# Performance work log

Measured on AMD Instinct MI355X. Metric: run time of the kernel, lower is better.

## Reference

```python
import jax, jax.numpy as jnp
from jax import lax
import numpy as np


def hac_round(X, W):
    """Avg-linkage HAC build+cut rounding of fractional SDP matrix X (D,D).
    Returns the 0/1 symmetric round_matrix with 1-diagonal."""
    D = X.shape[0]
    dt = X.dtype
    MAXD = jnp.max(jnp.abs(X)) * 1000.0  # _MAX_DIST sentinel
    max_sim = jnp.max(X)                 # max_similarity passed by forward()
    tril_mask = jnp.tril(jnp.ones((D, D), dtype=bool))
    # use_similarities=True branch: Y = MAXD*tril + (max_sim - X).triu(1)
    Y = jnp.where(tril_mask, MAXD, max_sim - X)
    values = jnp.min(Y, axis=1)
    indices = jnp.argmin(Y, axis=1)
    parents = jnp.arange(2 * D - 1)
    p2i = jnp.arange(2 * D - 1)   # parent_to_idx
    i2p = jnp.arange(D)           # idx_to_parent
    cs = jnp.ones(2 * D - 1, dtype=dt)
    energy = jnp.zeros(2 * D - 1, dtype=dt)
    clustering = jnp.zeros((2 * D - 1, D), dtype=dt)
    clustering = clustering.at[jnp.arange(D), jnp.arange(D)].set(jnp.arange(1, D + 1, dtype=dt))
    R = jnp.eye(D, dtype=dt)

    def body(i, st):
        Y, values, indices, parents, p2i, i2p, cs, energy, clustering, R = st
        max_node = D + i
        m1 = jnp.argmin(values)
        m2 = indices[m1]
        p1 = i2p[p2i[i2p[m1]]]
        p2 = i2p[p2i[i2p[m2]]]
        parents = parents.at[p1].set(max_node).at[p2].set(max_node)
        i2p = i2p.at[m1].set(max_node)
        p2i = p2i.at[max_node].set(m1)
        max_mask = Y == MAXD
        cs1, cs2 = cs[p1], cs[p2]
        ncs = cs1 + cs2
        cs = cs.at[max_node].set(ncs)
        # weighted average-linkage merged distances
        newv = (jnp.minimum(Y[m1, :], Y[:, m1]) * cs1 + jnp.minimum(Y[:, m2], Y[m2, :]) * cs2) / ncs
        Y = Y.at[:, m1].set(newv).at[m1, :].set(newv)
        Y = jnp.where(max_mask, MAXD, Y)
        Y = Y.at[:, m2].set(MAXD).at[m2, :].set(MAXD)
        values = values.at[m2].set(MAXD)
        vmask = values == MAXD
        values = jnp.where(vmask, MAXD, jnp.min(Y, axis=1))
        indices = jnp.argmin(Y, axis=1)
        # cut decision for the new internal node
        crow = clustering[p1] + clustering[p2]
        leaf = crow > 0                      # membership of new cluster
        lf = leaf.astype(dt)
        merge_e = lf @ (W @ lf)              # sum of W over leaf x leaf pairs
        e_sum = energy[p1] + energy[p2]
        take = merge_e >= e_sum
        energy = energy.at[max_node].set(jnp.where(take, merge_e, e_sum))
        crow = jnp.where(take & leaf, (max_node).astype(dt), crow)
        clustering = clustering.at[max_node].set(crow)
        R = jnp.where(take & (leaf[:, None] & leaf[None, :]), jnp.asarray(1.0, dt), R)
        return (Y, values, indices, parents, p2i, i2p, cs, energy, clustering, R)

    st = (Y, values, indices, parents, p2i, i2p, cs, energy, clustering, R)
    st = lax.fori_loop(0, D - 1, body, st)
    return st[-1]


def setup_inputs() -> dict:
    key = jax.random.key(0)
    k1, k2 = jax.random.split(key)
    D = 1024
    A = jax.random.uniform(k1, (D, D), dtype=jnp.float32)
    X = 0.5 * (A + A.T)                      # symmetric fractional decisions
    X = X.at[jnp.arange(D), jnp.arange(D)].set(1.0)  # 1-diagonal
    W = jnp.triu(jax.random.normal(k2, (D, D), dtype=jnp.float32), 1)  # triu(1) weights
    return {"X": X, "W": W}


def reference(X, W):
    # straight-through estimator: hard rounded solution, identity gradient w.r.t. X
    R = hac_round(X, W)
    return X + lax.stop_gradient(R - X)
```

## Files before the change

### kernel.cpp

```cpp
#include <hip/hip_runtime.h>
#include <stdint.h>

#define D 1024

typedef unsigned long long u64;
typedef unsigned int u32;

__device__ __forceinline__ u32 enc_f(float f) {
    u32 b = __float_as_uint(f);
    return (b & 0x80000000u) ? ~b : (b | 0x80000000u);
}
__device__ __forceinline__ float dec_f(u32 u) {
    u32 b = (u & 0x80000000u) ? (u ^ 0x80000000u) : ~u;
    return __uint_as_float(b);
}

__device__ __forceinline__ void barrier_lds_only() {
    __builtin_amdgcn_sched_barrier(0);
    asm volatile("s_waitcnt lgkmcnt(0)" ::: "memory");
    __builtin_amdgcn_s_barrier();
    asm volatile("" ::: "memory");
    __builtin_amdgcn_sched_barrier(0);
}

__global__ void k_maxred(const float* __restrict__ X, u32* scal) {
    float mx = -INFINITY, ma = 0.f;
    int stride = gridDim.x * blockDim.x;
    for (int i = blockIdx.x * blockDim.x + threadIdx.x; i < D * D; i += stride) {
        float v = X[i];
        mx = fmaxf(mx, v);
        ma = fmaxf(ma, fabsf(v));
    }
    for (int o = 32; o; o >>= 1) {
        mx = fmaxf(mx, __shfl_xor(mx, o));
        ma = fmaxf(ma, __shfl_xor(ma, o));
    }
    if ((threadIdx.x & 63) == 0) {
        atomicMax(&scal[0], enc_f(mx));
        atomicMax(&scal[1], enc_f(ma));
    }
}

__global__ void k_init(const float* __restrict__ X, const float* __restrict__ W,
                       float2* __restrict__ dc, const u32* __restrict__ scal) {
    int idx = blockIdx.x * blockDim.x + threadIdx.x;
    if (idx >= D * D) return;
    float max_sim = dec_f(scal[0]);
    float MAXD = __fmul_rn(dec_f(scal[1]), 1000.0f);
    int i = idx >> 10, j = idx & (D - 1);
    float x = X[idx];
    float di = (i == j) ? MAXD : __fsub_rn(max_sim, x);
    float cx = (i == j) ? 0.0f : (W[idx] + W[j * D + i]);
    dc[idx] = make_float2(di, cx);
}

__global__ void k_rowmin(const float2* __restrict__ dc, float* __restrict__ values_g,
                         int* __restrict__ indices_g, const u32* __restrict__ scal) {
    int r = blockIdx.x;
    int lane = threadIdx.x;
    float MAXD = __fmul_rn(dec_f(scal[1]), 1000.0f);
    u64 best = ((u64)__float_as_uint(MAXD) << 32);
    const float4* row4 = (const float4*)(dc + (size_t)r * D);
    for (int c = lane; c < D / 2; c += 64) {
        float4 q = row4[c];
        int j0 = c << 1;
        if (j0 > r) {
            u64 k = ((u64)__float_as_uint(q.x) << 32) | (u32)j0;
            if (k < best) best = k;
        }
        if (j0 + 1 > r) {
            u64 k = ((u64)__float_as_uint(q.z) << 32) | (u32)(j0 + 1);
            if (k < best) best = k;
        }
    }
    for (int o = 32; o; o >>= 1) {
        u64 k2 = __shfl_xor(best, o);
        if (k2 < best) best = k2;
    }
    if (lane == 0) {
        values_g[r] = __uint_as_float((u32)(best >> 32));
        indices_g[r] = (int)(best & 0xffffffffu);
    }
}

__global__ void __launch_bounds__(1024) k_hac(
        float2* __restrict__ dc,
        const float* __restrict__ values_g, const int* __restrict__ indices_g,
        int* __restrict__ labels_g, const u32* __restrict__ scal) {
    __shared__ __align__(16) float values_l[D];
    __shared__ float values_stage[D];
    __shared__ int indices_l[D];
    __shared__ __align__(16) float newv_l[D];
    __shared__ float cs_l[D];
    __shared__ unsigned char dead_l[D];
    __shared__ unsigned char marked_l[D];
    __shared__ int slot_l[D];
    __shared__ int label_l[D];
    __shared__ double within_l[D];
    __shared__ double energy_l[D];
    __shared__ int rlist[2][D];
    __shared__ int nrec[2];
    __shared__ u64 s_best[2];
    __shared__ float s_cross12;
    __shared__ int s_takeP, s_m1P, s_labP;

    const int t = threadIdx.x;
    const int lane = t & 63, wid = t >> 6;
    const float MAXD = __fmul_rn(dec_f(scal[1]), 1000.0f);
    const u32 MAXDb = __float_as_uint(MAXD);

    values_l[t] = values_g[t];
    indices_l[t] = indices_g[t];
    cs_l[t] = 1.0f;
    dead_l[t] = 0;
    marked_l[t] = 0;
    slot_l[t] = t;
    label_l[t] = t;
    within_l[t] = 0.0;
    energy_l[t] = 0.0;
    if (t == 0) {
        s_takeP = 0; s_m1P = -1; s_labP = 0;
        nrec[0] = 0; nrec[1] = 0;
        s_best[0] = ~0ull; s_best[1] = ~0ull;
    }
    __syncthreads();
    {
        u64 key = ((u64)__float_as_uint(values_l[t]) << 32) | ((u32)t << 10) |
                  (u32)indices_l[t];
        for (int o = 32; o; o >>= 1) {
            u64 k2 = __shfl_xor(key, o);
            if (k2 < key) key = k2;
        }
        if (lane == 0) atomicMin(&s_best[0], key);
    }
    __syncthreads();

    float pf0 = 0.f, pf1 = 0.f, pf2 = 0.f, pf3 = 0.f;

    for (int it = 0; it < D - 1; ++it) {
        const int cb = it & 1, pb = cb ^ 1;

        const u64 bk = s_best[cb];
        const int m1 = (int)((bk >> 10) & 1023);
        const int m2 = (int)(bk & 1023);

        const float2 v1 = dc[(size_t)m1 * D + t];
        const float2 v2 = dc[(size_t)m2 * D + t];

        const float cs1 = cs_l[m1], cs2 = cs_l[m2];
        const float ncs = __fadd_rn(cs1, cs2);
        const int pm1 = s_m1P;
        const int takeP = s_takeP, labP = s_labP;
        if (t == 0) s_best[pb] = ~0ull;

        if (marked_l[t]) { values_l[t] = values_stage[t]; marked_l[t] = 0; }
        if (t == m2) {
            dead_l[m2] = 1;
            values_l[m2] = MAXD;
            indices_l[m2] = 0;
        }
        const bool alive = !dead_l[t];

        const float d1 = v1.x, c1 = v1.y, d2 = v2.x, c2 = v2.y;

        {
            int sl = slot_l[t];
            if (takeP && sl == pm1) label_l[t] = labP;
            if (sl == m2) slot_l[t] = m1;
        }

        float nv = MAXD, ncx = 0.0f;
        bool do_st = false;
        if (t == m2) s_cross12 = c1;
        if (alive && t != m1) {
            nv = __fdiv_rn(__fadd_rn(__fmul_rn(d1, cs1), __fmul_rn(d2, cs2)), ncs);
            ncx = c1 + c2;
            dc[(size_t)m1 * D + t] = make_float2(nv, ncx);
            do_st = true;
        }
        newv_l[t] = nv;

        {
            float v = values_l[t];
            if (t == m1) {
                values_l[t] = MAXD;
                marked_l[t] = 1;
            } else if (alive && v < MAXD) {
                int idx = indices_l[t];
                if (idx == m2) {
                    rlist[cb][atomicAdd(&nrec[cb], 1)] = t;
                    values_l[t] = MAXD;
                    marked_l[t] = 1;
                } else if (idx == m1) {
                    if (nv <= v) values_l[t] = nv;
                    else {
                        rlist[cb][atomicAdd(&nrec[cb], 1)] = t;
                        values_l[t] = MAXD;
                        marked_l[t] = 1;
                    }
                } else if (t < m1) {
                    if (nv < v) { values_l[t] = nv; indices_l[t] = m1; }
                    else if (nv == v && m1 < idx) indices_l[t] = m1;
                }
            }
        }
        barrier_lds_only();

        if (t == m1) cs_l[m1] = ncs;
        const int n = nrec[cb];
        if (t == 0) nrec[pb] = 0;

        if (wid == 0) {
            if (do_st) dc[(size_t)t * D + m1] = make_float2(nv, ncx);
            if (lane == 0) {
                double merge_e = within_l[m1] + within_l[m2] + (double)s_cross12;
                double e_sum = energy_l[m1] + energy_l[m2];
                int take = (merge_e >= e_sum) ? 1 : 0;
                within_l[m1] = merge_e;
                energy_l[m1] = take ? merge_e : e_sum;
                s_takeP = take;
                s_m1P = m1;
                s_labP = D + it;
            }
            const float4* v4 = (const float4*)values_l;
            u64 bb = ~0ull;
#pragma unroll
            for (int c = 0; c < 4; ++c) {
                int fi = lane + 64 * c;
                float4 q = v4[fi];
                int b = fi << 2;
                u64 k;
                k = ((u64)__float_as_uint(q.x) << 32) | (u32)(b + 0); if (k < bb) bb = k;
                k = ((u64)__float_as_uint(q.y) << 32) | (u32)(b + 1); if (k < bb) bb = k;
                k = ((u64)__float_as_uint(q.z) << 32) | (u32)(b + 2); if (k < bb) bb = k;
                k = ((u64)__float_as_uint(q.w) << 32) | (u32)(b + 3); if (k < bb) bb = k;
            }
            for (int o = 32; o; o >>= 1) {
                u64 k2 = __shfl_xor(bb, o);
                if (k2 < bb) bb = k2;
            }
            if (lane == 0) {
                int r = (int)(bb & 1023);
                int idx = indices_l[r];
                atomicMin(&s_best[pb],
                          (bb & 0xffffffff00000000ull) | ((u32)r << 10) | (u32)idx);
            }
            {
                int r_pf = (int)(bb & 1023);
                int i_pf = indices_l[r_pf];
                const float* br = (const float*)(dc + (size_t)r_pf * D);
                const float* bi = (const float*)(dc + (size_t)i_pf * D);
                pf0 = br[lane * 16];
                pf1 = br[1024 + lane * 16];
                pf2 = bi[lane * 16];
                pf3 = bi[1024 + lane * 16];
            }
        } else if (wid == 1) {
            if (do_st) dc[(size_t)t * D + m1] = make_float2(nv, ncx);
            u64 bb = ((u64)MAXDb << 32);
            const float4* nv4 = (const float4*)newv_l;
            for (int c = lane; c < D / 4; c += 64) {
                float4 q = nv4[c];
                int j0 = c << 2;
#pragma unroll
                for (int e = 0; e < 4; ++e) {
                    int j = j0 + e;
                    float dv = (e == 0) ? q.x : (e == 1) ? q.y : (e == 2) ? q.z : q.w;
                    if (j > m1) {
                        u64 k = ((u64)__float_as_uint(dv) << 32) | (u32)j;
                        if (k < bb) bb = k;
                    }
                }
            }
            for (int o = 32; o; o >>= 1) {
                u64 k2 = __shfl_xor(bb, o);
                if (k2 < bb) bb = k2;
            }
            if (lane == 0) {
                values_stage[m1] = __uint_as_float((u32)(bb >> 32));
                indices_l[m1] = (int)(bb & 0xffffffffu);
                atomicMin(&s_best[pb],
                          (bb & 0xffffffff00000000ull) | ((u32)m1 << 10) | (bb & 1023));
            }
        } else {
            bool pend_st = do_st;
            for (int q = wid - 2; q < n; q += 14) {
                const int r = rlist[cb][q];
                const float subst = newv_l[r];
                const float4* row4 = (const float4*)(dc + (size_t)r * D);
                float4 a0 = row4[lane];
                float4 a1 = row4[lane + 64];
                float4 a2 = row4[lane + 128];
                float4 a3 = row4[lane + 192];
                float4 a4 = row4[lane + 256];
                float4 a5 = row4[lane + 320];
                float4 a6 = row4[lane + 384];
                float4 a7 = row4[lane + 448];
                if (pend_st) {
                    dc[(size_t)t * D + m1] = make_float2(nv, ncx);
                    pend_st = false;
                }
                u64 bb = ((u64)MAXDb << 32);
#define ACC2(af, koff)                                                          \
                {                                                               \
                    int j0 = (lane + (koff)) << 1;                              \
                    float dv0 = (j0 == m1) ? subst : (af).x;                    \
                    if (j0 > r && !dead_l[j0]) {                                \
                        u64 k = ((u64)__float_as_uint(dv0) << 32) | (u32)j0;    \
                        if (k < bb) bb = k;                                     \
                    }                                                           \
                    int j1 = j0 + 1;                                            \
                    float dv1 = (j1 == m1) ? subst : (af).z;                    \
                    if (j1 > r && !dead_l[j1]) {                                \
                        u64 k = ((u64)__float_as_uint(dv1) << 32) | (u32)j1;    \
                        if (k < bb) bb = k;                                     \
                    }                                                           \
                }
                ACC2(a0, 0)
                ACC2(a1, 64)
                ACC2(a2, 128)
                ACC2(a3, 192)
                ACC2(a4, 256)
                ACC2(a5, 320)
                ACC2(a6, 384)
                ACC2(a7, 448)
#undef ACC2
                for (int o = 32; o; o >>= 1) {
                    u64 k2 = __shfl_xor(bb, o);
                    if (k2 < bb) bb = k2;
                }
                if (lane == 0) {
                    values_stage[r] = __uint_as_float((u32)(bb >> 32));
                    indices_l[r] = (int)(bb & 0xffffffffu);
                    atomicMin(&s_best[pb],
                              (bb & 0xffffffff00000000ull) | ((u32)r << 10) | (bb & 1023));
                }
            }
            if (pend_st) dc[(size_t)t * D + m1] = make_float2(nv, ncx);
        }
        __syncthreads();
        if (wid == 0) asm volatile("" :: "v"(pf0), "v"(pf1), "v"(pf2), "v"(pf3));
    }

    {
        int lab = label_l[t];
        if (s_takeP && slot_l[t] == s_m1P) lab = s_labP;
        labels_g[t] = lab;
    }
}

__global__ void k_out(const int* __restrict__ labels, float* __restrict__ out) {
    int idx = blockIdx.x * blockDim.x + threadIdx.x;
    if (idx >= D * D) return;
    int i = idx >> 10, j = idx & (D - 1);
    out[idx] = (i == j || labels[i] == labels[j]) ? 1.0f : 0.0f;
}

extern "C" void kernel_launch(void* const* d_in, const int* in_sizes, int n_in,
                              void* d_out, int out_size, void* d_ws, size_t ws_size,
                              hipStream_t stream) {
    const float* X = (const float*)d_in[0];
    const float* W = (const float*)d_in[1];

    char* ws = (char*)d_ws;
    const size_t MAT_BYTES = (size_t)D * D * sizeof(float);
    float2* dc = (float2*)ws;
    float* values_g = (float*)(ws + 2 * MAT_BYTES);
    int* indices_g = (int*)(ws + 2 * MAT_BYTES + 4096);
    int* labels_g = (int*)(ws + 2 * MAT_BYTES + 8192);
    u32* scal = (u32*)(ws + 2 * MAT_BYTES + 12288);

    hipMemsetAsync(scal, 0, 2 * sizeof(u32), stream);
    k_maxred<<<256, 256, 0, stream>>>(X, scal);
    k_init<<<(D * D) / 256, 256, 0, stream>>>(X, W, dc, scal);
    k_rowmin<<<D, 64, 0, stream>>>(dc, values_g, indices_g, scal);
    k_hac<<<1, 1024, 0, stream>>>(dc, values_g, indices_g, labels_g, scal);
    k_out<<<(D * D) / 256, 256, 0, stream>>>(labels_g, (float*)d_out);
}
```

Measured before the change: 3.032 ms.

## Keep per-row HAC state in registers and distribute argmin across all waves

Per-row values, indices, marked, dead, slot and label state move from LDS arrays into per-thread registers. Every wave now folds its own rows into the next-iteration best key with a shuffle reduction and an atomicMin before the barrier. Previously wave 0 scanned the whole values array after the barrier, so this shortens the serial critical path of each merge iteration. In exchange the custom LDS-only barrier becomes a full __syncthreads, and the prefetch now reads a best key that later recomputed rows may still change.

```diff
diff --git a/kernel.cpp b/kernel.cpp
--- a/kernel.cpp
+++ b/kernel.cpp
@@ -13,14 +13,6 @@
 __device__ __forceinline__ float dec_f(u32 u) {
     u32 b = (u & 0x80000000u) ? (u ^ 0x80000000u) : ~u;
     return __uint_as_float(b);
-}
-
-__device__ __forceinline__ void barrier_lds_only() {
-    __builtin_amdgcn_sched_barrier(0);
-    asm volatile("s_waitcnt lgkmcnt(0)" ::: "memory");
-    __builtin_amdgcn_s_barrier();
-    asm volatile("" ::: "memory");
-    __builtin_amdgcn_sched_barrier(0);
 }
 
 __global__ void k_maxred(const float* __restrict__ X, u32* scal) {
@@ -87,21 +79,17 @@
         float2* __restrict__ dc,
         const float* __restrict__ values_g, const int* __restrict__ indices_g,
         int* __restrict__ labels_g, const u32* __restrict__ scal) {
-    __shared__ __align__(16) float values_l[D];
     __shared__ float values_stage[D];
     __shared__ int indices_l[D];
     __shared__ __align__(16) float newv_l[D];
     __shared__ float cs_l[D];
     __shared__ unsigned char dead_l[D];
-    __shared__ unsigned char marked_l[D];
-    __shared__ int slot_l[D];
-    __shared__ int label_l[D];
-    __shared__ double within_l[D];
-    __shared__ double energy_l[D];
     __shared__ int rlist[2][D];
     __shared__ int nrec[2];
     __shared__ u64 s_best[2];
     __shared__ float s_cross12;
+    __shared__ double within_l[D];
+    __shared__ double energy_l[D];
     __shared__ int s_takeP, s_m1P, s_labP;
 
     const int t = threadIdx.x;
@@ -109,13 +97,17 @@
     const float MAXD = __fmul_rn(dec_f(scal[1]), 1000.0f);
     const u32 MAXDb = __float_as_uint(MAXD);
 
-    values_l[t] = values_g[t];
-    indices_l[t] = indices_g[t];
+    float vreg = values_g[t];
+    int ireg = indices_g[t];
+    int mreg = 0;
+    int dreg = 0;
+    int sreg = t;
+    int lreg = t;
+
+    values_stage[t] = vreg;
+    indices_l[t] = ireg;
     cs_l[t] = 1.0f;
     dead_l[t] = 0;
-    marked_l[t] = 0;
-    slot_l[t] = t;
-    label_l[t] = t;
     within_l[t] = 0.0;
     energy_l[t] = 0.0;
     if (t == 0) {
@@ -125,8 +117,7 @@
     }
     __syncthreads();
     {
-        u64 key = ((u64)__float_as_uint(values_l[t]) << 32) | ((u32)t << 10) |
-                  (u32)indices_l[t];
+        u64 key = ((u64)__float_as_uint(vreg) << 32) | ((u32)t << 10) | (u32)ireg;
         for (int o = 32; o; o >>= 1) {
             u64 k2 = __shfl_xor(key, o);
             if (k2 < key) key = k2;
@@ -148,26 +139,26 @@
         const float2 v2 = dc[(size_t)m2 * D + t];
 
         const float cs1 = cs_l[m1], cs2 = cs_l[m2];
-        const float ncs = __fadd_rn(cs1, cs2);
+        const float v_stg = values_stage[t];
+        const int i_stg = indices_l[t];
         const int pm1 = s_m1P;
         const int takeP = s_takeP, labP = s_labP;
-        if (t == 0) s_best[pb] = ~0ull;
-
-        if (marked_l[t]) { values_l[t] = values_stage[t]; marked_l[t] = 0; }
+
+        const float ncs = __fadd_rn(cs1, cs2);
+
+        if (mreg) { vreg = v_stg; ireg = i_stg; mreg = 0; }
         if (t == m2) {
+            dreg = 1;
             dead_l[m2] = 1;
-            values_l[m2] = MAXD;
-            indices_l[m2] = 0;
-        }
-        const bool alive = !dead_l[t];
+            vreg = MAXD;
+            ireg = 0;
+        }
+        const bool alive = !dreg;
 
         const float d1 = v1.x, c1 = v1.y, d2 = v2.x, c2 = v2.y;
 
-        {
-            int sl = slot_l[t];
-            if (takeP && sl == pm1) label_l[t] = labP;
-            if (sl == m2) slot_l[t] = m1;
-        }
+        if (takeP && sreg == pm1) lreg = labP;
+        if (sreg == m2) sreg = m1;
 
         float nv = MAXD, ncx = 0.0f;
         bool do_st = false;
@@ -181,34 +172,42 @@
         newv_l[t] = nv;
 
         {
-            float v = values_l[t];
+            const float v = vreg;
             if (t == m1) {
-                values_l[t] = MAXD;
-                marked_l[t] = 1;
+                vreg = MAXD;
+                mreg = 1;
             } else if (alive && v < MAXD) {
-                int idx = indices_l[t];
-                if (idx == m2) {
+                if (ireg == m2) {
                     rlist[cb][atomicAdd(&nrec[cb], 1)] = t;
-                    values_l[t] = MAXD;
-                    marked_l[t] = 1;
-                } else if (idx == m1) {
-                    if (nv <= v) values_l[t] = nv;
+                    vreg = MAXD; mreg = 1;
+                } else if (ireg == m1) {
+                    if (nv <= v) vreg = nv;
                     else {
                         rlist[cb][atomicAdd(&nrec[cb], 1)] = t;
-                        values_l[t] = MAXD;
-                        marked_l[t] = 1;
+                        vreg = MAXD; mreg = 1;
                     }
                 } else if (t < m1) {
-                    if (nv < v) { values_l[t] = nv; indices_l[t] = m1; }
-                    else if (nv == v && m1 < idx) indices_l[t] = m1;
-                }
-            }
-        }
-        barrier_lds_only();
+                    if (nv < v) { vreg = nv; ireg = m1; }
+                    else if (nv == v && m1 < ireg) ireg = m1;
+                }
+            }
+        }
+        {
+            u64 key = ((u64)__float_as_uint(vreg) << 32) | ((u32)t << 10) | (u32)ireg;
+            for (int o = 32; o; o >>= 1) {
+                u64 k2 = __shfl_xor(key, o);
+                if (k2 < key) key = k2;
+            }
+            if (lane == 0) atomicMin(&s_best[pb], key);
+        }
+        __syncthreads();
 
         if (t == m1) cs_l[m1] = ncs;
         const int n = nrec[cb];
-        if (t == 0) nrec[pb] = 0;
+        if (t == 0) {
+            nrec[pb] = 0;
+            s_best[cb] = ~0ull;
+        }
 
         if (wid == 0) {
             if (do_st) dc[(size_t)t * D + m1] = make_float2(nv, ncx);
@@ -222,32 +221,10 @@
                 s_m1P = m1;
                 s_labP = D + it;
             }
-            const float4* v4 = (const float4*)values_l;
-            u64 bb = ~0ull;
-#pragma unroll
-            for (int c = 0; c < 4; ++c) {
-                int fi = lane + 64 * c;
-                float4 q = v4[fi];
-                int b = fi << 2;
-                u64 k;
-                k = ((u64)__float_as_uint(q.x) << 32) | (u32)(b + 0); if (k < bb) bb = k;
-                k = ((u64)__float_as_uint(q.y) << 32) | (u32)(b + 1); if (k < bb) bb = k;
-                k = ((u64)__float_as_uint(q.z) << 32) | (u32)(b + 2); if (k < bb) bb = k;
-                k = ((u64)__float_as_uint(q.w) << 32) | (u32)(b + 3); if (k < bb) bb = k;
-            }
-            for (int o = 32; o; o >>= 1) {
-                u64 k2 = __shfl_xor(bb, o);
-                if (k2 < bb) bb = k2;
-            }
-            if (lane == 0) {
-                int r = (int)(bb & 1023);
-                int idx = indices_l[r];
-                atomicMin(&s_best[pb],
-                          (bb & 0xffffffff00000000ull) | ((u32)r << 10) | (u32)idx);
-            }
             {
-                int r_pf = (int)(bb & 1023);
-                int i_pf = indices_l[r_pf];
+                const u64 cand = s_best[pb];
+                int r_pf = (int)((cand >> 10) & 1023);
+                int i_pf = (int)(cand & 1023);
                 const float* br = (const float*)(dc + (size_t)r_pf * D);
                 const float* bi = (const float*)(dc + (size_t)i_pf * D);
                 pf0 = br[lane * 16];
@@ -343,8 +320,8 @@
     }
 
     {
-        int lab = label_l[t];
-        if (s_takeP && slot_l[t] == s_m1P) lab = s_labP;
+        int lab = lreg;
+        if (s_takeP && sreg == s_m1P) lab = s_labP;
         labels_g[t] = lab;
     }
 }
```

Result: slower. 3.566 ms (+17.6%).

## Track second-best neighbor per row to avoid full row-min rescans

Applied to the files above, without the earlier changes.

Each row now keeps both the smallest and second-smallest (value, index) candidates, computed in the initial row-min pass and in every rescan via a top-2 warp reduction. When a row's best neighbor is merged away or worsens, the kernel falls back to the cached second-best instead of queuing the row for a full rescan. The aim is fewer rescans per iteration on the serial single-block HAC loop. In exchange the reductions do more work, more LDS is used, and the update logic becomes harder to keep exactly tie-equivalent to the reference.

```diff
diff --git a/kernel.cpp b/kernel.cpp
--- a/kernel.cpp
+++ b/kernel.cpp
@@ -54,41 +54,54 @@
     dc[idx] = make_float2(di, cx);
 }
 
-__global__ void k_rowmin(const float2* __restrict__ dc, float* __restrict__ values_g,
-                         int* __restrict__ indices_g, const u32* __restrict__ scal) {
+__global__ void k_rowmin(const float2* __restrict__ dc,
+                         float* __restrict__ values_g, int* __restrict__ indices_g,
+                         float* __restrict__ values2_g, int* __restrict__ indices2_g,
+                         const u32* __restrict__ scal) {
     int r = blockIdx.x;
     int lane = threadIdx.x;
     float MAXD = __fmul_rn(dec_f(scal[1]), 1000.0f);
-    u64 best = ((u64)__float_as_uint(MAXD) << 32);
+    const u32 MAXDb = __float_as_uint(MAXD);
+    u64 b1 = ((u64)MAXDb << 32);
+    u64 b2 = ((u64)MAXDb << 32) | 1023ull;
     const float4* row4 = (const float4*)(dc + (size_t)r * D);
     for (int c = lane; c < D / 2; c += 64) {
         float4 q = row4[c];
         int j0 = c << 1;
         if (j0 > r) {
             u64 k = ((u64)__float_as_uint(q.x) << 32) | (u32)j0;
-            if (k < best) best = k;
+            if (k < b1) { b2 = b1; b1 = k; } else if (k < b2) b2 = k;
         }
         if (j0 + 1 > r) {
             u64 k = ((u64)__float_as_uint(q.z) << 32) | (u32)(j0 + 1);
-            if (k < best) best = k;
+            if (k < b1) { b2 = b1; b1 = k; } else if (k < b2) b2 = k;
         }
     }
     for (int o = 32; o; o >>= 1) {
-        u64 k2 = __shfl_xor(best, o);
-        if (k2 < best) best = k2;
+        u64 c1 = __shfl_xor(b1, o), c2 = __shfl_xor(b2, o);
+        u64 lo = (b1 < c1) ? b1 : c1;
+        u64 hi = (b1 < c1) ? c1 : b1;
+        u64 mn2 = (b2 < c2) ? b2 : c2;
+        u64 sec = (hi < mn2) ? hi : mn2;
+        b1 = lo; b2 = sec;
     }
     if (lane == 0) {
-        values_g[r] = __uint_as_float((u32)(best >> 32));
-        indices_g[r] = (int)(best & 0xffffffffu);
+        values_g[r] = __uint_as_float((u32)(b1 >> 32));
+        indices_g[r] = (int)(b1 & 0xffffffffu);
+        values2_g[r] = __uint_as_float((u32)(b2 >> 32));
+        indices2_g[r] = (int)(b2 & 0xffffffffu);
     }
 }
 
 __global__ void __launch_bounds__(1024) k_hac(
         float2* __restrict__ dc,
         const float* __restrict__ values_g, const int* __restrict__ indices_g,
+        const float* __restrict__ values2_g, const int* __restrict__ indices2_g,
         int* __restrict__ labels_g, const u32* __restrict__ scal) {
     __shared__ __align__(16) float values_l[D];
     __shared__ float values_stage[D];
+    __shared__ float stage2_v[D];
+    __shared__ int stage2_i[D];
     __shared__ int indices_l[D];
     __shared__ __align__(16) float newv_l[D];
     __shared__ float cs_l[D];
@@ -109,8 +122,14 @@
     const float MAXD = __fmul_rn(dec_f(scal[1]), 1000.0f);
     const u32 MAXDb = __float_as_uint(MAXD);
 
+    float v2reg = values2_g[t];
+    int i2reg = indices2_g[t];
+
     values_l[t] = values_g[t];
     indices_l[t] = indices_g[t];
+    values_stage[t] = values_l[t];
+    stage2_v[t] = v2reg;
+    stage2_i[t] = i2reg;
     cs_l[t] = 1.0f;
     dead_l[t] = 0;
     marked_l[t] = 0;
@@ -145,29 +164,38 @@
         const int m2 = (int)(bk & 1023);
 
         const float2 v1 = dc[(size_t)m1 * D + t];
-        const float2 v2 = dc[(size_t)m2 * D + t];
+        const float2 v2g = dc[(size_t)m2 * D + t];
 
         const float cs1 = cs_l[m1], cs2 = cs_l[m2];
-        const float ncs = __fadd_rn(cs1, cs2);
+        const float v_std = values_l[t];
+        const float v_stg = values_stage[t];
+        const float s2v = stage2_v[t];
+        const int s2i = stage2_i[t];
+        const int mk = marked_l[t];
+        const int dd = dead_l[t];
+        int idx = indices_l[t];
+        const int sl = slot_l[t];
         const int pm1 = s_m1P;
         const int takeP = s_takeP, labP = s_labP;
         if (t == 0) s_best[pb] = ~0ull;
 
-        if (marked_l[t]) { values_l[t] = values_stage[t]; marked_l[t] = 0; }
+        const float ncs = __fadd_rn(cs1, cs2);
+
+        float v = mk ? v_stg : v_std;
+        if (mk) { values_l[t] = v; marked_l[t] = 0; v2reg = s2v; i2reg = s2i; }
         if (t == m2) {
             dead_l[m2] = 1;
             values_l[m2] = MAXD;
             indices_l[m2] = 0;
-        }
-        const bool alive = !dead_l[t];
-
-        const float d1 = v1.x, c1 = v1.y, d2 = v2.x, c2 = v2.y;
-
-        {
-            int sl = slot_l[t];
-            if (takeP && sl == pm1) label_l[t] = labP;
-            if (sl == m2) slot_l[t] = m1;
-        }
+            v = MAXD;
+            idx = 0;
+        }
+        const bool alive = !dd && (t != m2);
+
+        const float d1 = v1.x, c1 = v1.y, d2 = v2g.x, c2 = v2g.y;
+
+        if (takeP && sl == pm1) label_l[t] = labP;
+        if (sl == m2) slot_l[t] = m1;
 
         float nv = MAXD, ncx = 0.0f;
         bool do_st = false;
@@ -180,28 +208,49 @@
         }
         newv_l[t] = nv;
 
-        {
-            float v = values_l[t];
-            if (t == m1) {
+        if (t == m1) {
+            values_l[t] = MAXD;
+            marked_l[t] = 1;
+        } else if (alive && v < MAXD) {
+            if (v2reg < MAXD && i2reg == m2) v2reg = MAXD;
+            const bool v2ok = (v2reg < MAXD);
+            const u64 kn = ((u64)__float_as_uint(nv) << 32) | (u32)m1;
+            const u64 kv2 = ((u64)__float_as_uint(v2reg) << 32) | (u32)i2reg;
+            bool resc = false;
+            if (idx == m2) {
+                if (!v2ok) resc = true;
+                else if (i2reg == m1) {
+                    if (nv < v2reg) { values_l[t] = nv; indices_l[t] = m1; v2reg = MAXD; }
+                    else resc = true;
+                } else if (t < m1) {
+                    if (kn < kv2) { values_l[t] = nv; indices_l[t] = m1; }
+                    else { values_l[t] = v2reg; indices_l[t] = i2reg; v2reg = MAXD; }
+                } else {
+                    values_l[t] = v2reg; indices_l[t] = i2reg; v2reg = MAXD;
+                }
+            } else if (idx == m1) {
+                if (nv <= v) {
+                    values_l[t] = nv;
+                } else if (v2ok) {
+                    if (kn < kv2) values_l[t] = nv;
+                    else { values_l[t] = v2reg; indices_l[t] = i2reg; v2reg = MAXD; }
+                } else resc = true;
+            } else if (t < m1) {
+                const u64 kv1 = ((u64)__float_as_uint(v) << 32) | (u32)idx;
+                if (kn < kv1) {
+                    values_l[t] = nv; indices_l[t] = m1;
+                    v2reg = v; i2reg = idx;
+                } else if (v2ok) {
+                    if (i2reg == m1) {
+                        if (nv <= v2reg) v2reg = nv;
+                        else v2reg = MAXD;
+                    } else if (kn < kv2) { v2reg = nv; i2reg = m1; }
+                }
+            }
+            if (resc) {
+                rlist[cb][atomicAdd(&nrec[cb], 1)] = t;
                 values_l[t] = MAXD;
                 marked_l[t] = 1;
-            } else if (alive && v < MAXD) {
-                int idx = indices_l[t];
-                if (idx == m2) {
-                    rlist[cb][atomicAdd(&nrec[cb], 1)] = t;
-                    values_l[t] = MAXD;
-                    marked_l[t] = 1;
-                } else if (idx == m1) {
-                    if (nv <= v) values_l[t] = nv;
-                    else {
-                        rlist[cb][atomicAdd(&nrec[cb], 1)] = t;
-                        values_l[t] = MAXD;
-                        marked_l[t] = 1;
-                    }
-                } else if (t < m1) {
-                    if (nv < v) { values_l[t] = nv; indices_l[t] = m1; }
-                    else if (nv == v && m1 < idx) indices_l[t] = m1;
-                }
             }
         }
         barrier_lds_only();
@@ -241,9 +290,9 @@
             }
             if (lane == 0) {
                 int r = (int)(bb & 1023);
-                int idx = indices_l[r];
+                int idx2 = indices_l[r];
                 atomicMin(&s_best[pb],
-                          (bb & 0xffffffff00000000ull) | ((u32)r << 10) | (u32)idx);
+                          (bb & 0xffffffff00000000ull) | ((u32)r << 10) | (u32)idx2);
             }
             {
                 int r_pf = (int)(bb & 1023);
@@ -257,7 +306,8 @@
             }
         } else if (wid == 1) {
             if (do_st) dc[(size_t)t * D + m1] = make_float2(nv, ncx);
-            u64 bb = ((u64)MAXDb << 32);
+            u64 b1 = ((u64)MAXDb << 32);
+            u64 b2 = ((u64)MAXDb << 32) | 1023ull;
             const float4* nv4 = (const float4*)newv_l;
             for (int c = lane; c < D / 4; c += 64) {
                 float4 q = nv4[c];
@@ -268,19 +318,25 @@
                     float dv = (e == 0) ? q.x : (e == 1) ? q.y : (e == 2) ? q.z : q.w;
                     if (j > m1) {
                         u64 k = ((u64)__float_as_uint(dv) << 32) | (u32)j;
-                        if (k < bb) bb = k;
+                        if (k < b1) { b2 = b1; b1 = k; } else if (k < b2) b2 = k;
                     }
                 }
             }
             for (int o = 32; o; o >>= 1) {
-                u64 k2 = __shfl_xor(bb, o);
-                if (k2 < bb) bb = k2;
+                u64 c1k = __shfl_xor(b1, o), c2k = __shfl_xor(b2, o);
+                u64 lo = (b1 < c1k) ? b1 : c1k;
+                u64 hi = (b1 < c1k) ? c1k : b1;
+                u64 mn2 = (b2 < c2k) ? b2 : c2k;
+                u64 sec = (hi < mn2) ? hi : mn2;
+                b1 = lo; b2 = sec;
             }
             if (lane == 0) {
-                values_stage[m1] = __uint_as_float((u32)(bb >> 32));
-                indices_l[m1] = (int)(bb & 0xffffffffu);
+                values_stage[m1] = __uint_as_float((u32)(b1 >> 32));
+                indices_l[m1] = (int)(b1 & 0xffffffffu);
+                stage2_v[m1] = __uint_as_float((u32)(b2 >> 32));
+                stage2_i[m1] = (int)(b2 & 0xffffffffu);
                 atomicMin(&s_best[pb],
-                          (bb & 0xffffffff00000000ull) | ((u32)m1 << 10) | (bb & 1023));
+                          (b1 & 0xffffffff00000000ull) | ((u32)m1 << 10) | (b1 & 1023));
             }
         } else {
             bool pend_st = do_st;
@@ -300,20 +356,21 @@
                     dc[(size_t)t * D + m1] = make_float2(nv, ncx);
                     pend_st = false;
                 }
-                u64 bb = ((u64)MAXDb << 32);
+                u64 b1 = ((u64)MAXDb << 32);
+                u64 b2 = ((u64)MAXDb << 32) | 1023ull;
 #define ACC2(af, koff)                                                          \
                 {                                                               \
                     int j0 = (lane + (koff)) << 1;                              \
                     float dv0 = (j0 == m1) ? subst : (af).x;                    \
                     if (j0 > r && !dead_l[j0]) {                                \
                         u64 k = ((u64)__float_as_uint(dv0) << 32) | (u32)j0;    \
-                        if (k < bb) bb = k;                                     \
+                        if (k < b1) { b2 = b1; b1 = k; } else if (k < b2) b2 = k;\
                     }                                                           \
                     int j1 = j0 + 1;                                            \
                     float dv1 = (j1 == m1) ? subst : (af).z;                    \
                     if (j1 > r && !dead_l[j1]) {                                \
                         u64 k = ((u64)__float_as_uint(dv1) << 32) | (u32)j1;    \
-                        if (k < bb) bb = k;                                     \
+                        if (k < b1) { b2 = b1; b1 = k; } else if (k < b2) b2 = k;\
                     }                                                           \
                 }
                 ACC2(a0, 0)
@@ -326,14 +383,20 @@
                 ACC2(a7, 448)
 #undef ACC2
                 for (int o = 32; o; o >>= 1) {
-                    u64 k2 = __shfl_xor(bb, o);
-                    if (k2 < bb) bb = k2;
+                    u64 c1k = __shfl_xor(b1, o), c2k = __shfl_xor(b2, o);
+                    u64 lo = (b1 < c1k) ? b1 : c1k;
+                    u64 hi = (b1 < c1k) ? c1k : b1;
+                    u64 mn2 = (b2 < c2k) ? b2 : c2k;
+                    u64 sec = (hi < mn2) ? hi : mn2;
+                    b1 = lo; b2 = sec;
                 }
                 if (lane == 0) {
-                    values_stage[r] = __uint_as_float((u32)(bb >> 32));
-                    indices_l[r] = (int)(bb & 0xffffffffu);
+                    values_stage[r] = __uint_as_float((u32)(b1 >> 32));
+                    indices_l[r] = (int)(b1 & 0xffffffffu);
+                    stage2_v[r] = __uint_as_float((u32)(b2 >> 32));
+                    stage2_i[r] = (int)(b2 & 0xffffffffu);
                     atomicMin(&s_best[pb],
-                              (bb & 0xffffffff00000000ull) | ((u32)r << 10) | (bb & 1023));
+                              (b1 & 0xffffffff00000000ull) | ((u32)r << 10) | (b1 & 1023));
                 }
             }
             if (pend_st) dc[(size_t)t * D + m1] = make_float2(nv, ncx);
@@ -369,11 +432,14 @@
     int* indices_g = (int*)(ws + 2 * MAT_BYTES + 4096);
     int* labels_g = (int*)(ws + 2 * MAT_BYTES + 8192);
     u32* scal = (u32*)(ws + 2 * MAT_BYTES + 12288);
+    float* values2_g = (float*)(ws + 2 * MAT_BYTES + 16384);
+    int* indices2_g = (int*)(ws + 2 * MAT_BYTES + 20480);
 
     hipMemsetAsync(scal, 0, 2 * sizeof(u32), stream);
     k_maxred<<<256, 256, 0, stream>>>(X, scal);
     k_init<<<(D * D) / 256, 256, 0, stream>>>(X, W, dc, scal);
-    k_rowmin<<<D, 64, 0, stream>>>(dc, values_g, indices_g, scal);
-    k_hac<<<1, 1024, 0, stream>>>(dc, values_g, indices_g, labels_g, scal);
+    k_rowmin<<<D, 64, 0, stream>>>(dc, values_g, indices_g, values2_g, indices2_g, scal);
+    k_hac<<<1, 1024, 0, stream>>>(dc, values_g, indices_g, values2_g, indices2_g,
+                                  labels_g, scal);
     k_out<<<(D * D) / 256, 256, 0, stream>>>(labels_g, (float*)d_out);
 }
```

Result: slower. 3.340 ms (+10.2%).
